# Kernel tuning notes

Measured on AMD Instinct MI355X. Metric: run time of the kernel, lower is better.

The kernel has to match this reference:

```python
import jax, jax.numpy as jnp
import numpy as np


def setup_inputs() -> dict:
    key = jax.random.key(0)
    k1, k2 = jax.random.split(key)
    x = jax.random.normal(k1, (4, 2048, 2048), dtype=jnp.float32)
    weight = jax.random.normal(k2, (8192, 2048), dtype=jnp.float32) * 0.02
    return {"x": x, "weight": weight, "bits": 8}


def reference(x, weight, bits):
    # ---- activation quantization (per-row int8-style) ----
    scale = jnp.clip(jnp.max(jnp.abs(x), axis=-1, keepdims=True), 1e-5)  # [..., 1]
    max_val = (1 << (bits - 1)) - 1  # 127 for 8 bits
    x_q = jnp.clip(jnp.round(x * (max_val / scale)), -max_val, max_val)

    # ---- ternary weight quantization (-1, 0, 1) ----
    w_scale = jnp.mean(jnp.abs(weight))
    w_q = jnp.where(weight > 0.5 * w_scale, 1.0, 0.0) + jnp.where(
        weight < -0.5 * w_scale, -1.0, 0.0
    )

    # ---- dequantized linear: (x_q @ (w_q * w_scale)^T) / x_scale ----
    out = jnp.einsum("bsi,oi->bso", x_q, w_q * w_scale) / scale

    # ---- squared ReLU ----
    return jnp.maximum(out, 0.0) ** 2
```

## Files before the change

kernel.cpp:

```cpp
#include <hip/hip_runtime.h>
#include <hip/hip_bf16.h>

typedef __attribute__((ext_vector_type(4))) int i32x4;
typedef __attribute__((ext_vector_type(16))) int i32x16;

#define M_DIM 8192
#define N_DIM 8192
#define K_DIM 2048
#define WCOUNT (N_DIM * K_DIM)


__global__ __launch_bounds__(256) void k_abs_partial(const float* __restrict__ w,
                                                     float* __restrict__ part) {
    int tid = blockIdx.x * 256 + threadIdx.x;
    const float4* w4 = (const float4*)w;
    float s = 0.0f;
    const int total4 = WCOUNT / 4;
    for (int i = tid; i < total4; i += 2048 * 256) {
        float4 v = w4[i];
        s += fabsf(v.x) + fabsf(v.y) + fabsf(v.z) + fabsf(v.w);
    }
    #pragma unroll
    for (int off = 1; off < 64; off <<= 1) s += __shfl_xor(s, off);
    __shared__ float red[4];
    if ((threadIdx.x & 63) == 0) red[threadIdx.x >> 6] = s;
    __syncthreads();
    if (threadIdx.x == 0)
        part[blockIdx.x] = (red[0] + red[1]) + (red[2] + red[3]);
}

__global__ __launch_bounds__(256) void k_abs_final(const float* __restrict__ part,
                                                   float* __restrict__ sum) {
    int t = threadIdx.x;
    float s = 0.0f;
    #pragma unroll
    for (int i = 0; i < 8; i++) s += part[t + i * 256];
    #pragma unroll
    for (int off = 1; off < 64; off <<= 1) s += __shfl_xor(s, off);
    __shared__ float red[4];
    if ((t & 63) == 0) red[t >> 6] = s;
    __syncthreads();
    if (t == 0) sum[0] = (red[0] + red[1]) + (red[2] + red[3]);
}

__global__ __launch_bounds__(256) void k_wquant(const float* __restrict__ w,
                                                const float* __restrict__ sum,
                                                signed char* __restrict__ wqf) {
    const float thr = 0.5f * (sum[0] * (1.0f / 16777216.0f));
    const int g = blockIdx.x * 256 + threadIdx.x;
    const int n = g >> 7;
    const int kc = g & 127;
    const float4* wr = (const float4*)(w + (size_t)n * K_DIM + kc * 16);
    union { signed char c[16]; uint4 v; } pk;
    #pragma unroll
    for (int q = 0; q < 4; q++) {
        float4 v = wr[q];
        pk.c[q * 4 + 0] = v.x > thr ? 1 : (v.x < -thr ? -1 : 0);
        pk.c[q * 4 + 1] = v.y > thr ? 1 : (v.y < -thr ? -1 : 0);
        pk.c[q * 4 + 2] = v.z > thr ? 1 : (v.z < -thr ? -1 : 0);
        pk.c[q * 4 + 3] = v.w > thr ? 1 : (v.w < -thr ? -1 : 0);
    }
    *(uint4*)(wqf + (size_t)(n >> 5) * 65536 + kc * 512 + (n & 31) * 16) = pk.v;
}

__global__ __launch_bounds__(256) void k_xquant(const float* __restrict__ x,
                                                signed char* __restrict__ xqf,
                                                float* __restrict__ scale) {
    const int row = blockIdx.x;
    const int t = threadIdx.x;
    const float4* xr = (const float4*)(x + (size_t)row * K_DIM);
    float4 a = xr[t * 2];
    float4 b = xr[t * 2 + 1];
    float m = fmaxf(fmaxf(fmaxf(fabsf(a.x), fabsf(a.y)), fmaxf(fabsf(a.z), fabsf(a.w))),
                    fmaxf(fmaxf(fabsf(b.x), fabsf(b.y)), fmaxf(fabsf(b.z), fabsf(b.w))));
    #pragma unroll
    for (int off = 1; off < 64; off <<= 1) m = fmaxf(m, __shfl_xor(m, off));
    __shared__ float red[4];
    if ((t & 63) == 0) red[t >> 6] = m;
    __syncthreads();
    m = fmaxf(fmaxf(red[0], red[1]), fmaxf(red[2], red[3]));
    const float sc = fmaxf(m, 1e-5f);
    if (t == 0) scale[row] = sc;
    const float r = 127.0f / sc;
    float q[8] = {a.x, a.y, a.z, a.w, b.x, b.y, b.z, b.w};
    union { signed char c[8]; uint2 v; } pk;
    #pragma unroll
    for (int j = 0; j < 8; j++) {
        float v = rintf(q[j] * r);
        v = fminf(fmaxf(v, -127.0f), 127.0f);
        pk.c[j] = (signed char)v;
    }
    *(uint2*)(xqf + (size_t)(row >> 5) * 65536 + (t >> 1) * 512
              + (row & 31) * 16 + (t & 1) * 8) = pk.v;
}

__global__ __launch_bounds__(256) void k_coef(const float* __restrict__ sum,
                                              const float* __restrict__ scale,
                                              float* __restrict__ coef) {
    const int i = blockIdx.x * 256 + threadIdx.x;
    coef[i] = (sum[0] * (1.0f / 16777216.0f)) / scale[i];
}

#define GLDS16(g, l)                                                                   \
    __builtin_amdgcn_global_load_lds((const __attribute__((address_space(1))) void*)(g), \
                                     (__attribute__((address_space(3))) void*)(l), 16, 0, 0)

#define BAR __builtin_amdgcn_s_barrier()
#define VMCNT5 asm volatile("s_waitcnt vmcnt(5)" ::: "memory")
#define VMCNT4 asm volatile("s_waitcnt vmcnt(4)" ::: "memory")

__global__ __launch_bounds__(512, 4) void k_gemm(const signed char* __restrict__ xqf,
                                                 const signed char* __restrict__ wqf,
                                                 const float* __restrict__ coef,
                                                 float* __restrict__ out) {
    __shared__ signed char lds[16384];

    const int t = threadIdx.x;
    const int lane = t & 63;
    const int wid = t >> 6;
    const int wm = wid >> 2;
    const int wn = wid & 3;
    const int l31 = lane & 31;
    const int kg = lane >> 5;

    const int bid = blockIdx.x;
    const int xcd = bid & 7;
    const int idx = bid >> 3;
    const int bcol = (idx >> 5) * 4 + (idx & 3);
    const int brow = xcd * 8 + ((idx >> 2) & 7);

    const signed char* aSrc = xqf + (size_t)(brow * 4 + (t >> 7)) * 65536
                              + ((t >> 5) & 3) * 512 + (t & 31) * 16;
    const int aDst = wid * 1024;

    const signed char* bSrc = wqf + (size_t)(bcol * 8 + wn * 2) * 65536 + lane * 16;

    const int aRd = wm * 4096 + lane * 16;

    i32x16 acc00 = (i32x16){0,0,0,0,0,0,0,0,0,0,0,0,0,0,0,0};
    i32x16 acc01 = acc00, acc10 = acc00, acc11 = acc00;

#define STG_A(buf, kt) GLDS16(aSrc + (size_t)(kt) * 2048, lds + (buf) * 8192 + aDst)
#define LOADB(B0, B1, B2, B3, kt) do {                                             \
        B0 = *(const i32x4*)(bSrc + (size_t)(kt) * 2048);                          \
        B1 = *(const i32x4*)(bSrc + (size_t)(kt) * 2048 + 65536);                  \
        B2 = *(const i32x4*)(bSrc + (size_t)(kt) * 2048 + 1024);                   \
        B3 = *(const i32x4*)(bSrc + (size_t)(kt) * 2048 + 66560); } while (0)
#define HALF(buf, B0, B1, B2, B3) do {                                             \
        i32x4 a0 = *(const i32x4*)&lds[(buf) * 8192 + aRd];                        \
        i32x4 a1 = *(const i32x4*)&lds[(buf) * 8192 + aRd + 2048];                 \
        __builtin_amdgcn_s_setprio(1);                                             \
        acc00 = __builtin_amdgcn_mfma_i32_32x32x32_i8(a0, B0, acc00, 0, 0, 0);     \
        acc01 = __builtin_amdgcn_mfma_i32_32x32x32_i8(a0, B1, acc01, 0, 0, 0);     \
        acc10 = __builtin_amdgcn_mfma_i32_32x32x32_i8(a1, B0, acc10, 0, 0, 0);     \
        acc11 = __builtin_amdgcn_mfma_i32_32x32x32_i8(a1, B1, acc11, 0, 0, 0);     \
        __builtin_amdgcn_s_setprio(0);                                             \
        a0 = *(const i32x4*)&lds[(buf) * 8192 + aRd + 1024];                       \
        a1 = *(const i32x4*)&lds[(buf) * 8192 + aRd + 3072];                       \
        __builtin_amdgcn_s_setprio(1);                                             \
        acc00 = __builtin_amdgcn_mfma_i32_32x32x32_i8(a0, B2, acc00, 0, 0, 0);     \
        acc01 = __builtin_amdgcn_mfma_i32_32x32x32_i8(a0, B3, acc01, 0, 0, 0);     \
        acc10 = __builtin_amdgcn_mfma_i32_32x32x32_i8(a1, B2, acc10, 0, 0, 0);     \
        acc11 = __builtin_amdgcn_mfma_i32_32x32x32_i8(a1, B3, acc11, 0, 0, 0);     \
        __builtin_amdgcn_s_setprio(0); } while (0)

    i32x4 BA0, BA1, BA2, BA3, BB0, BB1, BB2, BB3;

    STG_A(0, 0);
    STG_A(1, 1);
    LOADB(BA0, BA1, BA2, BA3, 0);
    VMCNT5;
    BAR;

    #pragma unroll 1
    for (int j = 0; j < 15; j++) {
        const int kt = 2 * j;
        LOADB(BB0, BB1, BB2, BB3, kt + 1);
        HALF(0, BA0, BA1, BA2, BA3);
        BAR;
        STG_A(0, kt + 2);
        VMCNT5;
        BAR;
        LOADB(BA0, BA1, BA2, BA3, kt + 2);
        HALF(1, BB0, BB1, BB2, BB3);
        BAR;
        STG_A(1, kt + 3);
        VMCNT5;
        BAR;
    }
    LOADB(BB0, BB1, BB2, BB3, 31);
    HALF(0, BA0, BA1, BA2, BA3);
    BAR;
    VMCNT4;
    BAR;
    HALF(1, BB0, BB1, BB2, BB3);

    const int rb = brow * 128 + wm * 64 + 4 * kg;
    const int cb = bcol * 256 + wn * 64 + l31;
    #pragma unroll
    for (int mt = 0; mt < 2; mt++) {
        const i32x16 ac0 = mt ? acc10 : acc00;
        const i32x16 ac1 = mt ? acc11 : acc01;
        #pragma unroll
        for (int r = 0; r < 16; r++) {
            const int grow = rb + mt * 32 + (r & 3) + 8 * (r >> 2);
            const float c = coef[grow];
            float v0 = (float)ac0[r] * c; v0 = fmaxf(v0, 0.0f);
            float v1 = (float)ac1[r] * c; v1 = fmaxf(v1, 0.0f);
            __builtin_nontemporal_store(v0 * v0, &out[(size_t)grow * N_DIM + cb]);
            __builtin_nontemporal_store(v1 * v1, &out[(size_t)grow * N_DIM + cb + 32]);
        }
    }
#undef STG_A
#undef LOADB
#undef HALF
}

extern "C" void kernel_launch(void* const* d_in, const int* in_sizes, int n_in,
                              void* d_out, int out_size, void* d_ws, size_t ws_size,
                              hipStream_t stream) {
    const float* x = (const float*)d_in[0];
    const float* w = (const float*)d_in[1];
    float* out = (float*)d_out;

    char* ws = (char*)d_ws;
    float* sum   = (float*)ws;
    float* part  = (float*)(ws + 256);
    float* scale = (float*)(ws + 16384);
    float* coef  = (float*)(ws + 49152);
    signed char* xqf = (signed char*)(ws + 131072);
    signed char* wqf = (signed char*)(ws + 131072 + 16777216);

    k_abs_partial<<<2048, 256, 0, stream>>>(w, part);
    k_abs_final<<<1, 256, 0, stream>>>(part, sum);
    k_wquant<<<4096, 256, 0, stream>>>(w, sum, wqf);
    k_xquant<<<M_DIM, 256, 0, stream>>>(x, xqf, scale);
    k_coef<<<32, 256, 0, stream>>>(sum, scale, coef);
    k_gemm<<<dim3(2048), 512, 0, stream>>>(xqf, wqf, coef, out);
}
```

Measured before the change: 203.9 us.

## Stage both A and B tiles through LDS with 128x128 tiles and triple buffering

The GEMM now moves both activation and weight tiles into LDS via global_load_lds, where before B fragments were loaded straight into registers. It uses a triple-buffered pipeline with a 3-deep prefetch. The block tile shrinks from 128x256 to 128x128 with 4 waves per block, and the grid doubles to 4096 blocks. The aim is deeper latency hiding and less register pressure, at the cost of more redundant global reads of A, since each block covers fewer columns, and more LDS per block.

Measured after the change: 196.7 us. 1.04x faster.

```diff
diff --git a/kernel.cpp b/kernel.cpp
--- a/kernel.cpp
+++ b/kernel.cpp
@@ -106,97 +106,98 @@
                                      (__attribute__((address_space(3))) void*)(l), 16, 0, 0)
 
 #define BAR __builtin_amdgcn_s_barrier()
-#define VMCNT5 asm volatile("s_waitcnt vmcnt(5)" ::: "memory")
-#define VMCNT4 asm volatile("s_waitcnt vmcnt(4)" ::: "memory")
-
-__global__ __launch_bounds__(512, 4) void k_gemm(const signed char* __restrict__ xqf,
+#define VMW(n) asm volatile("s_waitcnt vmcnt(" #n ")" ::: "memory")
+
+__global__ __launch_bounds__(256, 3) void k_gemm(const signed char* __restrict__ xqf,
                                                  const signed char* __restrict__ wqf,
                                                  const float* __restrict__ coef,
                                                  float* __restrict__ out) {
-    __shared__ signed char lds[16384];
+    __shared__ signed char lds[49152];
 
     const int t = threadIdx.x;
     const int lane = t & 63;
     const int wid = t >> 6;
-    const int wm = wid >> 2;
-    const int wn = wid & 3;
+    const int wm = wid >> 1;
+    const int wn = wid & 1;
     const int l31 = lane & 31;
     const int kg = lane >> 5;
 
     const int bid = blockIdx.x;
     const int xcd = bid & 7;
     const int idx = bid >> 3;
-    const int bcol = (idx >> 5) * 4 + (idx & 3);
-    const int brow = xcd * 8 + ((idx >> 2) & 7);
-
-    const signed char* aSrc = xqf + (size_t)(brow * 4 + (t >> 7)) * 65536
-                              + ((t >> 5) & 3) * 512 + (t & 31) * 16;
-    const int aDst = wid * 1024;
-
-    const signed char* bSrc = wqf + (size_t)(bcol * 8 + wn * 2) * 65536 + lane * 16;
+    const int grp = idx >> 5;
+    const int w_ = idx & 31;
+    const int bcol = grp * 4 + (w_ & 3);
+    const int brow = xcd * 8 + ((w_ >> 2) & 7);
+
+    const signed char* aSrc0 = xqf + (size_t)(brow * 4 + (t >> 7)) * 65536 + (t & 127) * 16;
+    const signed char* aSrc1 = xqf + (size_t)(brow * 4 + 2 + (t >> 7)) * 65536 + (t & 127) * 16;
+    const signed char* bSrc0 = wqf + (size_t)(bcol * 4 + (t >> 7)) * 65536 + (t & 127) * 16;
+    const signed char* bSrc1 = wqf + (size_t)(bcol * 4 + 2 + (t >> 7)) * 65536 + (t & 127) * 16;
+    const int dst0 = wid * 1024;
+    const int dst1 = 4096 + wid * 1024;
+
+#define STG(bufc, kt) do {                                                         \
+        GLDS16(aSrc0 + (size_t)(kt) * 2048, lds + (bufc) * 16384 + dst0);          \
+        GLDS16(aSrc1 + (size_t)(kt) * 2048, lds + (bufc) * 16384 + dst1);          \
+        GLDS16(bSrc0 + (size_t)(kt) * 2048, lds + (bufc) * 16384 + 8192 + dst0);   \
+        GLDS16(bSrc1 + (size_t)(kt) * 2048, lds + (bufc) * 16384 + 8192 + dst1);   \
+    } while (0)
 
     const int aRd = wm * 4096 + lane * 16;
+    const int bRd = 8192 + wn * 4096 + lane * 16;
 
     i32x16 acc00 = (i32x16){0,0,0,0,0,0,0,0,0,0,0,0,0,0,0,0};
     i32x16 acc01 = acc00, acc10 = acc00, acc11 = acc00;
 
-#define STG_A(buf, kt) GLDS16(aSrc + (size_t)(kt) * 2048, lds + (buf) * 8192 + aDst)
-#define LOADB(B0, B1, B2, B3, kt) do {                                             \
-        B0 = *(const i32x4*)(bSrc + (size_t)(kt) * 2048);                          \
-        B1 = *(const i32x4*)(bSrc + (size_t)(kt) * 2048 + 65536);                  \
-        B2 = *(const i32x4*)(bSrc + (size_t)(kt) * 2048 + 1024);                   \
-        B3 = *(const i32x4*)(bSrc + (size_t)(kt) * 2048 + 66560); } while (0)
-#define HALF(buf, B0, B1, B2, B3) do {                                             \
-        i32x4 a0 = *(const i32x4*)&lds[(buf) * 8192 + aRd];                        \
-        i32x4 a1 = *(const i32x4*)&lds[(buf) * 8192 + aRd + 2048];                 \
+#define MMK(bufc) do {                                                             \
+        const int ab = (bufc) * 16384 + aRd;                                       \
+        const int bb = (bufc) * 16384 + bRd;                                       \
+        i32x4 a00 = *(const i32x4*)&lds[ab];                                       \
+        i32x4 a10 = *(const i32x4*)&lds[ab + 2048];                                \
+        i32x4 b00 = *(const i32x4*)&lds[bb];                                       \
+        i32x4 b10 = *(const i32x4*)&lds[bb + 2048];                                \
+        i32x4 a01 = *(const i32x4*)&lds[ab + 1024];                                \
+        i32x4 a11 = *(const i32x4*)&lds[ab + 3072];                                \
+        i32x4 b01 = *(const i32x4*)&lds[bb + 1024];                                \
+        i32x4 b11 = *(const i32x4*)&lds[bb + 3072];                                \
         __builtin_amdgcn_s_setprio(1);                                             \
-        acc00 = __builtin_amdgcn_mfma_i32_32x32x32_i8(a0, B0, acc00, 0, 0, 0);     \
-        acc01 = __builtin_amdgcn_mfma_i32_32x32x32_i8(a0, B1, acc01, 0, 0, 0);     \
-        acc10 = __builtin_amdgcn_mfma_i32_32x32x32_i8(a1, B0, acc10, 0, 0, 0);     \
-        acc11 = __builtin_amdgcn_mfma_i32_32x32x32_i8(a1, B1, acc11, 0, 0, 0);     \
-        __builtin_amdgcn_s_setprio(0);                                             \
-        a0 = *(const i32x4*)&lds[(buf) * 8192 + aRd + 1024];                       \
-        a1 = *(const i32x4*)&lds[(buf) * 8192 + aRd + 3072];                       \
-        __builtin_amdgcn_s_setprio(1);                                             \
-        acc00 = __builtin_amdgcn_mfma_i32_32x32x32_i8(a0, B2, acc00, 0, 0, 0);     \
-        acc01 = __builtin_amdgcn_mfma_i32_32x32x32_i8(a0, B3, acc01, 0, 0, 0);     \
-        acc10 = __builtin_amdgcn_mfma_i32_32x32x32_i8(a1, B2, acc10, 0, 0, 0);     \
-        acc11 = __builtin_amdgcn_mfma_i32_32x32x32_i8(a1, B3, acc11, 0, 0, 0);     \
+        acc00 = __builtin_amdgcn_mfma_i32_32x32x32_i8(a00, b00, acc00, 0, 0, 0);   \
+        acc01 = __builtin_amdgcn_mfma_i32_32x32x32_i8(a00, b10, acc01, 0, 0, 0);   \
+        acc10 = __builtin_amdgcn_mfma_i32_32x32x32_i8(a10, b00, acc10, 0, 0, 0);   \
+        acc11 = __builtin_amdgcn_mfma_i32_32x32x32_i8(a10, b10, acc11, 0, 0, 0);   \
+        acc00 = __builtin_amdgcn_mfma_i32_32x32x32_i8(a01, b01, acc00, 0, 0, 0);   \
+        acc01 = __builtin_amdgcn_mfma_i32_32x32x32_i8(a01, b11, acc01, 0, 0, 0);   \
+        acc10 = __builtin_amdgcn_mfma_i32_32x32x32_i8(a11, b01, acc10, 0, 0, 0);   \
+        acc11 = __builtin_amdgcn_mfma_i32_32x32x32_i8(a11, b11, acc11, 0, 0, 0);   \
         __builtin_amdgcn_s_setprio(0); } while (0)
 
-    i32x4 BA0, BA1, BA2, BA3, BB0, BB1, BB2, BB3;
-
-    STG_A(0, 0);
-    STG_A(1, 1);
-    LOADB(BA0, BA1, BA2, BA3, 0);
-    VMCNT5;
+#define STEP(bufc, kt) do {                                                        \
+        MMK(bufc);                                                                 \
+        BAR;                                                                       \
+        STG(bufc, (kt) + 3);                                                       \
+        VMW(8);                                                                    \
+        BAR; } while (0)
+
+    STG(0, 0); STG(1, 1); STG(2, 2);
+    VMW(8);
     BAR;
 
     #pragma unroll 1
-    for (int j = 0; j < 15; j++) {
-        const int kt = 2 * j;
-        LOADB(BB0, BB1, BB2, BB3, kt + 1);
-        HALF(0, BA0, BA1, BA2, BA3);
-        BAR;
-        STG_A(0, kt + 2);
-        VMCNT5;
-        BAR;
-        LOADB(BA0, BA1, BA2, BA3, kt + 2);
-        HALF(1, BB0, BB1, BB2, BB3);
-        BAR;
-        STG_A(1, kt + 3);
-        VMCNT5;
-        BAR;
-    }
-    LOADB(BB0, BB1, BB2, BB3, 31);
-    HALF(0, BA0, BA1, BA2, BA3);
-    BAR;
-    VMCNT4;
-    BAR;
-    HALF(1, BB0, BB1, BB2, BB3);
+    for (int j = 0; j < 9; j++) {
+        const int kt = 3 * j;
+        STEP(0, kt);
+        STEP(1, kt + 1);
+        STEP(2, kt + 2);
+    }
+    STEP(0, 27);
+    STEP(1, 28);
+    MMK(2); BAR; VMW(4); BAR;
+    MMK(0); BAR; VMW(0); BAR;
+    MMK(1);
 
     const int rb = brow * 128 + wm * 64 + 4 * kg;
-    const int cb = bcol * 256 + wn * 64 + l31;
+    const int cb = bcol * 128 + wn * 64 + l31;
     #pragma unroll
     for (int mt = 0; mt < 2; mt++) {
         const i32x16 ac0 = mt ? acc10 : acc00;
@@ -211,9 +212,9 @@
             __builtin_nontemporal_store(v1 * v1, &out[(size_t)grow * N_DIM + cb + 32]);
         }
     }
-#undef STG_A
-#undef LOADB
-#undef HALF
+#undef STG
+#undef MMK
+#undef STEP
 }
 
 extern "C" void kernel_launch(void* const* d_in, const int* in_sizes, int n_in,
@@ -236,5 +237,5 @@
     k_wquant<<<4096, 256, 0, stream>>>(w, sum, wqf);
     k_xquant<<<M_DIM, 256, 0, stream>>>(x, xqf, scale);
     k_coef<<<32, 256, 0, stream>>>(sum, scale, coef);
-    k_gemm<<<dim3(2048), 512, 0, stream>>>(xqf, wqf, coef, out);
-}
+    k_gemm<<<dim3(4096), 256, 0, stream>>>(xqf, wqf, coef, out);
+}
```
